# Kernel optimization log

Measured on AMD Instinct MI355X. Metric: run time of the kernel, lower is better.

Reference implementation:

```python
import jax, jax.numpy as jnp
import numpy as np

B, N, E = 4, 50000, 800000
C_IN, C_OUT, K = 64, 64, 3  # K = max_degree
AVG_DEG = 16.0


def setup_inputs() -> dict:
    key = jax.random.key(0)
    k1, k2, k3, k4, k5 = jax.random.split(key, 5)
    x = jax.random.normal(k1, (B, N, C_IN), dtype=jnp.float32)
    lap_rows = jax.random.randint(k2, (E,), 0, N)
    lap_cols = jax.random.randint(k3, (E,), 0, N)
    # scale so ||L|| stays O(1) and the Chebyshev recursion is stable
    lap_vals = jax.random.normal(k4, (E,), dtype=jnp.float32) / AVG_DEG
    weights = jax.random.normal(k5, (K + 1, C_IN, C_OUT), dtype=jnp.float32) * 0.1
    bias = jnp.full((C_OUT,), 0.1, dtype=jnp.float32)
    return dict(x=x, lap_rows=lap_rows, lap_cols=lap_cols,
                lap_vals=lap_vals, weights=weights, bias=bias)


def reference(x, lap_rows, lap_cols, lap_vals, weights, bias):
    # Sparse L @ X via edge list: gather source rows, scale, scatter-add to dest rows.
    def spmm_one(xb):  # xb: [N, C]
        return jax.ops.segment_sum(lap_vals[:, None] * xb[lap_cols], lap_rows,
                                   num_segments=N)

    spmm = jax.vmap(spmm_one)  # [B, N, C] -> [B, N, C]

    Tx0 = x
    out = jnp.einsum('bnc,co->bno', Tx0, weights[0])
    Tx1 = spmm(Tx0)
    out = out + jnp.einsum('bnc,co->bno', Tx1, weights[1])
    for k in range(2, K + 1):
        Tx2 = 2.0 * spmm(Tx1) - Tx0
        out = out + jnp.einsum('bnc,co->bno', Tx2, weights[k])
        Tx0, Tx1 = Tx1, Tx2
    return jax.nn.relu(out + bias)
```

## Files before the change

kernel.cpp:

```cpp
#include <hip/hip_runtime.h>


#define N_NODES 50000
#define N_EDGES 800000
#define BATCH 4
#define CH 64
#define BN (N_NODES * CH)
#define ROWS_TOTAL (BATCH * N_NODES)
#define NB 782
#define EPB 8192
#define SCT_BLOCKS ((N_EDGES + EPB - 1) / EPB)
#define TOTC (NB * SCT_BLOCKS)
#define SCAN2_BLOCKS ((TOTC + 1023) / 1024)

typedef unsigned int uint;
typedef unsigned short ushort;
typedef unsigned char uchar;
typedef __attribute__((ext_vector_type(8))) short short8;
typedef __attribute__((ext_vector_type(4))) float f32x4;

__device__ __forceinline__ uint pack_bf16(float lo, float hi) {
  uint a = __float_as_uint(lo);
  uint b = __float_as_uint(hi);
  a = (a + 0x7fffu + ((a >> 16) & 1u)) >> 16;
  b = (b + 0x7fffu + ((b >> 16) & 1u)) >> 16;
  return a | (b << 16);
}
__device__ __forceinline__ ushort bf16one(float x) {
  uint a = __float_as_uint(x);
  a = (a + 0x7fffu + ((a >> 16) & 1u)) >> 16;
  return (ushort)a;
}
__device__ __forceinline__ uint q_u8(float v, float inv) {
  return (uint)((int)rintf(v * inv) + 128) & 0xffu;
}

__global__ __launch_bounds__(1024) void bucket_hist(const int* __restrict__ rows,
                                                    int* __restrict__ bcounts) {
  __shared__ int h[NB];
  for (int b = threadIdx.x; b < NB; b += 1024) h[b] = 0;
  __syncthreads();
  int base_e = blockIdx.x * EPB;
#pragma unroll
  for (int j = 0; j < EPB / 1024; ++j) {
    int e = base_e + j * 1024 + threadIdx.x;
    if (e < N_EDGES) atomicAdd(&h[rows[e] >> 6], 1);
  }
  __syncthreads();
  for (int b = threadIdx.x; b < NB; b += 1024)
    bcounts[(size_t)b * SCT_BLOCKS + blockIdx.x] = h[b];
}

__global__ __launch_bounds__(1024) void partial2(const int* __restrict__ bc,
                                                 int* __restrict__ bsums) {
  int t = blockIdx.x * 1024 + threadIdx.x;
  int v = (t < TOTC) ? bc[t] : 0;
#pragma unroll
  for (int off = 1; off < 64; off <<= 1) v += __shfl_xor(v, off, 64);
  __shared__ int ws[16];
  if ((threadIdx.x & 63) == 0) ws[threadIdx.x >> 6] = v;
  __syncthreads();
  if (threadIdx.x < 16) {
    int s = ws[threadIdx.x];
#pragma unroll
    for (int off = 1; off < 16; off <<= 1) s += __shfl_xor(s, off, 64);
    if (threadIdx.x == 0) bsums[blockIdx.x] = s;
  }
}

__global__ __launch_bounds__(128) void scanb2(const int* __restrict__ bsums,
                                              int* __restrict__ boff) {
  __shared__ int s[128];
  int tid = threadIdx.x;
  int v = (tid < SCAN2_BLOCKS) ? bsums[tid] : 0;
  s[tid] = v;
  __syncthreads();
  for (int off = 1; off < 128; off <<= 1) {
    int t = (tid >= off) ? s[tid - off] : 0;
    __syncthreads();
    s[tid] += t;
    __syncthreads();
  }
  boff[tid] = s[tid] - v;
}

__global__ __launch_bounds__(1024) void expand2(const int* __restrict__ bc,
                                                const int* __restrict__ boff,
                                                int* __restrict__ bases) {
  int t = blockIdx.x * 1024 + threadIdx.x;
  int tid = threadIdx.x;
  int v = (t < TOTC) ? bc[t] : 0;
  __shared__ int s[1024];
  s[tid] = v;
  __syncthreads();
  for (int off = 1; off < 1024; off <<= 1) {
    int tv = (tid >= off) ? s[tid - off] : 0;
    __syncthreads();
    s[tid] += tv;
    __syncthreads();
  }
  if (t < TOTC) bases[t] = boff[blockIdx.x] + s[tid] - v;
}

__global__ __launch_bounds__(1024) void bucket_scatter(const int* __restrict__ rows,
                                                       const int* __restrict__ cols,
                                                       const float* __restrict__ vals,
                                                       const int* __restrict__ bases,
                                                       uint2* __restrict__ staging) {
  __shared__ int lcur[NB];
  for (int b = threadIdx.x; b < NB; b += 1024)
    lcur[b] = bases[(size_t)b * SCT_BLOCKS + blockIdx.x];
  __syncthreads();
  int base_e = blockIdx.x * EPB;
#pragma unroll
  for (int j = 0; j < EPB / 1024; ++j) {
    int e = base_e + j * 1024 + threadIdx.x;
    if (e < N_EDGES) {
      int r = rows[e];
      int pos = atomicAdd(&lcur[r >> 6], 1);
      staging[pos] = make_uint2((uint)cols[e] | ((uint)(r & 63) << 20),
                                __float_as_uint(vals[e]));
    }
  }
}

__global__ __launch_bounds__(256) void bucket_finalize(const int* __restrict__ bases,
                                                       const uint2* __restrict__ staging,
                                                       uint2* __restrict__ pairs,
                                                       int* __restrict__ row_start) {
  int b = blockIdx.x;
  int seg0 = bases[(size_t)b * SCT_BLOCKS];
  int seg1 = (b == NB - 1) ? N_EDGES : bases[(size_t)(b + 1) * SCT_BLOCKS];
  __shared__ int hist[64];
  __shared__ int cur[64];
  if (threadIdx.x < 64) hist[threadIdx.x] = 0;
  __syncthreads();
  for (int i = seg0 + threadIdx.x; i < seg1; i += 256)
    atomicAdd(&hist[staging[i].x >> 20], 1);
  __syncthreads();
  if (threadIdx.x < 64) {
    int v = hist[threadIdx.x];
    int sc = v;
#pragma unroll
    for (int off = 1; off < 64; off <<= 1) {
      int t = __shfl_up(sc, off, 64);
      if (threadIdx.x >= (unsigned)off) sc += t;
    }
    int start = seg0 + sc - v;
    cur[threadIdx.x] = start;
    int r = b * 64 + threadIdx.x;
    if (r < N_NODES) row_start[r] = start;
    if (r == N_NODES) row_start[N_NODES] = N_EDGES;
  }
  __syncthreads();
  for (int i = seg0 + threadIdx.x; i < seg1; i += 256) {
    uint2 eu = staging[i];
    int rl = eu.x >> 20;
    int pos = atomicAdd(&cur[rl], 1);
    pairs[pos] = make_uint2(eu.x & 0xFFFFFu, eu.y);
  }
}

__global__ __launch_bounds__(256) void wprep_kernel(const float* __restrict__ w,
                                                    ushort* __restrict__ wtT) {
  int t = blockIdx.x * 256 + threadIdx.x;
  if (t >= 64 * 256) return;
  int o = t >> 8, k = t & 255, m = k >> 6, c = k & 63;
  int idx = c * 64 + o;
  float v;
  if (m == 0)      v = w[idx] - w[2 * 4096 + idx];
  else if (m == 1) v = w[4096 + idx] - 3.0f * w[3 * 4096 + idx];
  else if (m == 2) v = 2.0f * w[2 * 4096 + idx];
  else             v = 4.0f * w[3 * 4096 + idx];
  wtT[t] = bf16one(v);
}

__global__ __launch_bounds__(256) void cvt_kernel(const float* __restrict__ in,
                                                  uint* __restrict__ xu8w,
                                                  float* __restrict__ xsc) {
  int node = blockIdx.x * 4 + (threadIdx.x >> 6);
  int lane = threadIdx.x & 63;
  int b = lane >> 4;
  int c4 = (lane & 15) * 4;
  float4 v = *reinterpret_cast<const float4*>(in + (size_t)b * BN + (size_t)node * 64 + c4);
  float mx = fmaxf(fmaxf(fabsf(v.x), fabsf(v.y)), fmaxf(fabsf(v.z), fabsf(v.w)));
#pragma unroll
  for (int off = 1; off < 64; off <<= 1) mx = fmaxf(mx, __shfl_xor(mx, off, 64));
  float inv = mx > 0.f ? 127.0f / mx : 0.f;
  uint w8 = q_u8(v.x, inv) | (q_u8(v.y, inv) << 8) |
            (q_u8(v.z, inv) << 16) | (q_u8(v.w, inv) << 24);
  xu8w[(size_t)node * 64 + b * 16 + (lane & 15)] = w8;
  if (lane == 0) xsc[node] = mx * (1.0f / 127.0f);
}

__device__ __forceinline__ void fma16_u8(float acc[16], float& sm, float m,
                                         const uint4& w) {
  const uint arr[4] = {w.x, w.y, w.z, w.w};
#pragma unroll
  for (int t = 0; t < 4; ++t) {
    uint u = arr[t];
    acc[t * 4 + 0] = fmaf(m, (float)(u & 0xffu),         acc[t * 4 + 0]);
    acc[t * 4 + 1] = fmaf(m, (float)((u >> 8) & 0xffu),  acc[t * 4 + 1]);
    acc[t * 4 + 2] = fmaf(m, (float)((u >> 16) & 0xffu), acc[t * 4 + 2]);
    acc[t * 4 + 3] = fmaf(m, (float)(u >> 24),           acc[t * 4 + 3]);
  }
  sm += m;
}

__device__ __forceinline__ void spmm_body(const int* __restrict__ row_start,
                                          const uint2* __restrict__ pairs,
                                          const uchar* __restrict__ src,
                                          const float* __restrict__ ssc,
                                          uchar* __restrict__ dst,
                                          float* __restrict__ dsc) {
  int row = blockIdx.x * 4 + (threadIdx.x >> 6);
  int lane = threadIdx.x & 63;
  int q = lane >> 4;
  int ql = lane & 15;
  const uchar* sb = src + ql * 16;
  int s = row_start[row], e = row_start[row + 1];
  float acc[16];
  float sm = 0.f;
#pragma unroll
  for (int j = 0; j < 16; ++j) acc[j] = 0.f;
  int i = s;
  for (; i + 7 < e; i += 8) {
    uint2 pa = pairs[i + q];
    uint2 pb = pairs[i + 4 + q];
    uint4 qa = *reinterpret_cast<const uint4*>(sb + (size_t)pa.x * 256);
    uint4 qb = *reinterpret_cast<const uint4*>(sb + (size_t)pb.x * 256);
    float ma = __uint_as_float(pa.y) * ssc[pa.x];
    float mb = __uint_as_float(pb.y) * ssc[pb.x];
    fma16_u8(acc, sm, ma, qa);
    fma16_u8(acc, sm, mb, qb);
  }
  for (; i < e; i += 4) {
    if (i + q < e) {
      uint2 p0 = pairs[i + q];
      uint4 q0 = *reinterpret_cast<const uint4*>(sb + (size_t)p0.x * 256);
      fma16_u8(acc, sm, __uint_as_float(p0.y) * ssc[p0.x], q0);
    }
  }
#pragma unroll
  for (int j = 0; j < 16; ++j) {
    acc[j] += __shfl_xor(acc[j], 16, 64);
    acc[j] += __shfl_xor(acc[j], 32, 64);
  }
  sm += __shfl_xor(sm, 16, 64);
  sm += __shfl_xor(sm, 32, 64);
#pragma unroll
  for (int j = 0; j < 16; ++j) acc[j] = fmaf(-128.f, sm, acc[j]);
  float mx = 0.f;
#pragma unroll
  for (int j = 0; j < 16; ++j) mx = fmaxf(mx, fabsf(acc[j]));
#pragma unroll
  for (int off = 1; off < 16; off <<= 1) mx = fmaxf(mx, __shfl_xor(mx, off, 64));
  if (lane < 16) {
    float inv = mx > 0.f ? 127.0f / mx : 0.f;
    uint w[4];
#pragma unroll
    for (int t = 0; t < 4; ++t) {
      w[t] = q_u8(acc[t * 4 + 0], inv) | (q_u8(acc[t * 4 + 1], inv) << 8) |
             (q_u8(acc[t * 4 + 2], inv) << 16) | (q_u8(acc[t * 4 + 3], inv) << 24);
    }
    *reinterpret_cast<uint4*>(dst + (size_t)row * 256 + ql * 16) =
        make_uint4(w[0], w[1], w[2], w[3]);
    if (lane == 0) dsc[row] = mx * (1.0f / 127.0f);
  }
}

__global__ __launch_bounds__(256) void spmm_s1(const int* __restrict__ rs,
                                               const uint2* __restrict__ pr,
                                               const uchar* __restrict__ src,
                                               const float* __restrict__ ssc,
                                               uchar* __restrict__ dst,
                                               float* __restrict__ dsc) {
  spmm_body(rs, pr, src, ssc, dst, dsc);
}
__global__ __launch_bounds__(256) void spmm_s2(const int* __restrict__ rs,
                                               const uint2* __restrict__ pr,
                                               const uchar* __restrict__ src,
                                               const float* __restrict__ ssc,
                                               uchar* __restrict__ dst,
                                               float* __restrict__ dsc) {
  spmm_body(rs, pr, src, ssc, dst, dsc);
}
__global__ __launch_bounds__(256) void spmm_s3(const int* __restrict__ rs,
                                               const uint2* __restrict__ pr,
                                               const uchar* __restrict__ src,
                                               const float* __restrict__ ssc,
                                               uchar* __restrict__ dst,
                                               float* __restrict__ dsc) {
  spmm_body(rs, pr, src, ssc, dst, dsc);
}

__device__ __forceinline__ short8 dequant8_u8(uint2 q, float sc, float nb) {
  float f0 = fmaf((float)(q.x & 0xffu),         sc, nb);
  float f1 = fmaf((float)((q.x >> 8) & 0xffu),  sc, nb);
  float f2 = fmaf((float)((q.x >> 16) & 0xffu), sc, nb);
  float f3 = fmaf((float)(q.x >> 24),           sc, nb);
  float f4 = fmaf((float)(q.y & 0xffu),         sc, nb);
  float f5 = fmaf((float)((q.y >> 8) & 0xffu),  sc, nb);
  float f6 = fmaf((float)((q.y >> 16) & 0xffu), sc, nb);
  float f7 = fmaf((float)(q.y >> 24),           sc, nb);
  uint4 v = make_uint4(pack_bf16(f0, f1), pack_bf16(f2, f3),
                       pack_bf16(f4, f5), pack_bf16(f6, f7));
  return __builtin_bit_cast(short8, v);
}

__global__ __launch_bounds__(256) void gemm4_mfma(
    const uchar* __restrict__ A0u8, const float* __restrict__ A0sc,
    const uchar* __restrict__ A1u8, const float* __restrict__ A1sc,
    const uchar* __restrict__ A2u8, const float* __restrict__ A2sc,
    const uchar* __restrict__ A3u8, const float* __restrict__ A3sc,
    const uint* __restrict__ wtT,
    const float* __restrict__ bias, float* __restrict__ out) {
  __shared__ uint WS[64 * 132];
  __shared__ float bias_s[64];
  for (int w = threadIdx.x; w < 8192; w += 256)
    WS[(w >> 7) * 132 + (w & 127)] = wtT[w];
  if (threadIdx.x < 64) bias_s[threadIdx.x] = bias[threadIdx.x];
  __syncthreads();

  const int lane = threadIdx.x & 63;
  const int wv = threadIdx.x >> 6;
  const int r0 = blockIdx.x * 64 + wv * 16;
  const int c16 = lane & 15;
  const int hi = lane >> 4;

  const int ar = r0 + c16;
  const size_t arow_b = (size_t)ar * 64 + hi * 8;
  const int nd = ar >> 2;
  const float sc0 = A0sc[nd];
  const float sc1 = A1sc[nd];
  const float sc2 = A2sc[nd];
  const float sc3 = A3sc[nd];

  f32x4 acc[4] = {{0.f, 0.f, 0.f, 0.f}, {0.f, 0.f, 0.f, 0.f},
                  {0.f, 0.f, 0.f, 0.f}, {0.f, 0.f, 0.f, 0.f}};

#pragma unroll
  for (int ks = 0; ks < 8; ++ks) {
    const int m = ks >> 1;
    const uchar* Au = (m == 0) ? A0u8 : (m == 1) ? A1u8 : (m == 2) ? A2u8 : A3u8;
    const float sc = (m == 0) ? sc0 : (m == 1) ? sc1 : (m == 2) ? sc2 : sc3;
    uint2 qv = *reinterpret_cast<const uint2*>(Au + arow_b + (ks & 1) * 32);
    short8 afrag = dequant8_u8(qv, sc, -128.f * sc);
#pragma unroll
    for (int nt = 0; nt < 4; ++nt) {
      uint4 bv = *reinterpret_cast<const uint4*>(
          &WS[(nt * 16 + c16) * 132 + ks * 16 + hi * 4]);
      short8 bfrag = __builtin_bit_cast(short8, bv);
      acc[nt] = __builtin_amdgcn_mfma_f32_16x16x32_bf16(afrag, bfrag, acc[nt], 0, 0, 0);
    }
  }

#pragma unroll
  for (int nt = 0; nt < 4; ++nt) {
#pragma unroll
    for (int i = 0; i < 4; ++i) {
      int row = r0 + hi * 4 + i;
      int node = row >> 2, b = row & 3;
      int col = nt * 16 + c16;
      float v = acc[nt][i] + bias_s[col];
      out[(size_t)b * BN + (size_t)node * 64 + col] = fmaxf(v, 0.f);
    }
  }
}

extern "C" void kernel_launch(void* const* d_in, const int* in_sizes, int n_in,
                              void* d_out, int out_size, void* d_ws, size_t ws_size,
                              hipStream_t stream) {
  const float* x        = (const float*)d_in[0];
  const int*   lap_rows = (const int*)d_in[1];
  const int*   lap_cols = (const int*)d_in[2];
  const float* lap_vals = (const float*)d_in[3];
  const float* weights  = (const float*)d_in[4];
  const float* bias     = (const float*)d_in[5];
  float* out = (float*)d_out;

  char* ws = (char*)d_ws;
  size_t off = 0;
  auto alloc = [&](size_t bytes) {
    void* p = ws + off;
    off += (bytes + 255) & ~(size_t)255;
    return p;
  };
  int*    bcounts     = (int*)alloc((size_t)TOTC * 4);
  int*    bases       = (int*)alloc((size_t)TOTC * 4);
  int*    bsums       = (int*)alloc((size_t)128 * 4);
  int*    boff        = (int*)alloc((size_t)128 * 4);
  int*    row_start   = (int*)alloc((size_t)(N_NODES + 1) * 4);
  uint2*  pairs       = (uint2*)alloc((size_t)N_EDGES * 8);
  uint2*  staging     = (uint2*)alloc((size_t)N_EDGES * 8);
  ushort* wtT         = (ushort*)alloc((size_t)64 * 256 * 2);
  uchar*  xu8         = (uchar*)alloc((size_t)N_NODES * 256);
  uchar*  S1u         = (uchar*)alloc((size_t)N_NODES * 256);
  uchar*  S2u         = (uchar*)alloc((size_t)N_NODES * 256);
  uchar*  S3u         = (uchar*)alloc((size_t)N_NODES * 256);
  float*  xsc         = (float*)alloc((size_t)N_NODES * 4);
  float*  S1sc        = (float*)alloc((size_t)N_NODES * 4);
  float*  S2sc        = (float*)alloc((size_t)N_NODES * 4);
  float*  S3sc        = (float*)alloc((size_t)N_NODES * 4);
  (void)ws_size; (void)in_sizes; (void)n_in; (void)out_size;

  wprep_kernel<<<64, 256, 0, stream>>>(weights, wtT);
  cvt_kernel<<<N_NODES / 4, 256, 0, stream>>>(x, (uint*)xu8, xsc);
  bucket_hist<<<SCT_BLOCKS, 1024, 0, stream>>>(lap_rows, bcounts);
  partial2<<<SCAN2_BLOCKS, 1024, 0, stream>>>(bcounts, bsums);
  scanb2<<<1, 128, 0, stream>>>(bsums, boff);
  expand2<<<SCAN2_BLOCKS, 1024, 0, stream>>>(bcounts, boff, bases);
  bucket_scatter<<<SCT_BLOCKS, 1024, 0, stream>>>(lap_rows, lap_cols, lap_vals,
                                                  bases, staging);
  bucket_finalize<<<NB, 256, 0, stream>>>(bases, staging, pairs, row_start);

  const int spmm_blocks = N_NODES / 4;

  spmm_s1<<<spmm_blocks, 256, 0, stream>>>(row_start, pairs, xu8, xsc, S1u, S1sc);
  spmm_s2<<<spmm_blocks, 256, 0, stream>>>(row_start, pairs, S1u, S1sc, S2u, S2sc);
  spmm_s3<<<spmm_blocks, 256, 0, stream>>>(row_start, pairs, S2u, S2sc, S3u, S3sc);
  gemm4_mfma<<<ROWS_TOTAL / 64, 256, 0, stream>>>(xu8, xsc, S1u, S1sc, S2u, S2sc,
                                                  S3u, S3sc, (const uint*)wtT,
                                                  bias, out);
}
```

Before: 189.1 us.

## Fuse third SpMM stage with the MFMA output GEMM

The last Chebyshev SpMM is merged with the final weight GEMM. Each block computes S3 for its 4 nodes, keeps the result in LDS as bf16 without quantizing it, and runs the MFMA over x, S1, S2 and the on-chip S3. This removes one launch plus the write and re-read of the quantized S3 buffer. In exchange, each wave computes only one 16-column output tile per block and reads weights straight from global/L2 rather than a shared LDS copy, so MFMA efficiency drops and weight traffic rises.

```diff
diff --git a/kernel.cpp b/kernel.cpp
--- a/kernel.cpp
+++ b/kernel.cpp
@@ -285,14 +285,6 @@
                                                float* __restrict__ dsc) {
   spmm_body(rs, pr, src, ssc, dst, dsc);
 }
-__global__ __launch_bounds__(256) void spmm_s3(const int* __restrict__ rs,
-                                               const uint2* __restrict__ pr,
-                                               const uchar* __restrict__ src,
-                                               const float* __restrict__ ssc,
-                                               uchar* __restrict__ dst,
-                                               float* __restrict__ dsc) {
-  spmm_body(rs, pr, src, ssc, dst, dsc);
-}
 
 __device__ __forceinline__ short8 dequant8_u8(uint2 q, float sc, float nb) {
   float f0 = fmaf((float)(q.x & 0xffu),         sc, nb);
@@ -308,63 +300,104 @@
   return __builtin_bit_cast(short8, v);
 }
 
-__global__ __launch_bounds__(256) void gemm4_mfma(
-    const uchar* __restrict__ A0u8, const float* __restrict__ A0sc,
-    const uchar* __restrict__ A1u8, const float* __restrict__ A1sc,
-    const uchar* __restrict__ A2u8, const float* __restrict__ A2sc,
-    const uchar* __restrict__ A3u8, const float* __restrict__ A3sc,
-    const uint* __restrict__ wtT,
-    const float* __restrict__ bias, float* __restrict__ out) {
-  __shared__ uint WS[64 * 132];
-  __shared__ float bias_s[64];
-  for (int w = threadIdx.x; w < 8192; w += 256)
-    WS[(w >> 7) * 132 + (w & 127)] = wtT[w];
-  if (threadIdx.x < 64) bias_s[threadIdx.x] = bias[threadIdx.x];
-  __syncthreads();
-
+__global__ __launch_bounds__(256) void spmm_s3_gemm(
+    const int* __restrict__ row_start, const uint2* __restrict__ pairs,
+    const uchar* __restrict__ xu8, const float* __restrict__ xsc,
+    const uchar* __restrict__ S1u, const float* __restrict__ S1sc,
+    const uchar* __restrict__ S2u, const float* __restrict__ S2sc,
+    const uint* __restrict__ wtT, const float* __restrict__ bias,
+    float* __restrict__ out) {
+  __shared__ uint S3L[16 * 36];
+  const int nb = blockIdx.x * 4;
+  const int wv = threadIdx.x >> 6;
+  const int row = nb + wv;
   const int lane = threadIdx.x & 63;
-  const int wv = threadIdx.x >> 6;
-  const int r0 = blockIdx.x * 64 + wv * 16;
+  const int q = lane >> 4;
+  const int ql = lane & 15;
+
+  const uchar* sb = S2u + ql * 16;
+  int s = row_start[row], e = row_start[row + 1];
+  float acc[16];
+  float sm = 0.f;
+#pragma unroll
+  for (int j = 0; j < 16; ++j) acc[j] = 0.f;
+  int i = s;
+  for (; i + 7 < e; i += 8) {
+    uint2 pa = pairs[i + q];
+    uint2 pb = pairs[i + 4 + q];
+    uint4 qa = *reinterpret_cast<const uint4*>(sb + (size_t)pa.x * 256);
+    uint4 qb = *reinterpret_cast<const uint4*>(sb + (size_t)pb.x * 256);
+    float ma = __uint_as_float(pa.y) * S2sc[pa.x];
+    float mb = __uint_as_float(pb.y) * S2sc[pb.x];
+    fma16_u8(acc, sm, ma, qa);
+    fma16_u8(acc, sm, mb, qb);
+  }
+  for (; i < e; i += 4) {
+    if (i + q < e) {
+      uint2 p0 = pairs[i + q];
+      uint4 q0 = *reinterpret_cast<const uint4*>(sb + (size_t)p0.x * 256);
+      fma16_u8(acc, sm, __uint_as_float(p0.y) * S2sc[p0.x], q0);
+    }
+  }
+#pragma unroll
+  for (int j = 0; j < 16; ++j) {
+    acc[j] += __shfl_xor(acc[j], 16, 64);
+    acc[j] += __shfl_xor(acc[j], 32, 64);
+  }
+  sm += __shfl_xor(sm, 16, 64);
+  sm += __shfl_xor(sm, 32, 64);
+#pragma unroll
+  for (int j = 0; j < 16; ++j) acc[j] = fmaf(-128.f, sm, acc[j]);
+
+  if (lane < 16) {
+    int r = wv * 4 + (ql >> 2);
+    int w0 = (ql & 3) * 8;
+    uint wb[8];
+#pragma unroll
+    for (int t = 0; t < 8; ++t) wb[t] = pack_bf16(acc[2 * t], acc[2 * t + 1]);
+    *reinterpret_cast<uint4*>(&S3L[r * 36 + w0]) =
+        make_uint4(wb[0], wb[1], wb[2], wb[3]);
+    *reinterpret_cast<uint4*>(&S3L[r * 36 + w0 + 4]) =
+        make_uint4(wb[4], wb[5], wb[6], wb[7]);
+  }
+  __syncthreads();
+
   const int c16 = lane & 15;
   const int hi = lane >> 4;
-
-  const int ar = r0 + c16;
-  const size_t arow_b = (size_t)ar * 64 + hi * 8;
-  const int nd = ar >> 2;
-  const float sc0 = A0sc[nd];
-  const float sc1 = A1sc[nd];
-  const float sc2 = A2sc[nd];
-  const float sc3 = A3sc[nd];
-
-  f32x4 acc[4] = {{0.f, 0.f, 0.f, 0.f}, {0.f, 0.f, 0.f, 0.f},
-                  {0.f, 0.f, 0.f, 0.f}, {0.f, 0.f, 0.f, 0.f}};
-
+  const int gnode = nb + (c16 >> 2);
+  const int bb = c16 & 3;
+  const size_t abase = (size_t)gnode * 256 + bb * 64 + hi * 8;
+  const float sc0 = xsc[gnode];
+  const float sc1 = S1sc[gnode];
+  const float sc2 = S2sc[gnode];
+  const int ocol = wv * 16 + c16;
+
+  f32x4 accd = {0.f, 0.f, 0.f, 0.f};
 #pragma unroll
   for (int ks = 0; ks < 8; ++ks) {
-    const int m = ks >> 1;
-    const uchar* Au = (m == 0) ? A0u8 : (m == 1) ? A1u8 : (m == 2) ? A2u8 : A3u8;
-    const float sc = (m == 0) ? sc0 : (m == 1) ? sc1 : (m == 2) ? sc2 : sc3;
-    uint2 qv = *reinterpret_cast<const uint2*>(Au + arow_b + (ks & 1) * 32);
-    short8 afrag = dequant8_u8(qv, sc, -128.f * sc);
-#pragma unroll
-    for (int nt = 0; nt < 4; ++nt) {
-      uint4 bv = *reinterpret_cast<const uint4*>(
-          &WS[(nt * 16 + c16) * 132 + ks * 16 + hi * 4]);
-      short8 bfrag = __builtin_bit_cast(short8, bv);
-      acc[nt] = __builtin_amdgcn_mfma_f32_16x16x32_bf16(afrag, bfrag, acc[nt], 0, 0, 0);
-    }
-  }
-
-#pragma unroll
-  for (int nt = 0; nt < 4; ++nt) {
-#pragma unroll
-    for (int i = 0; i < 4; ++i) {
-      int row = r0 + hi * 4 + i;
-      int node = row >> 2, b = row & 3;
-      int col = nt * 16 + c16;
-      float v = acc[nt][i] + bias_s[col];
-      out[(size_t)b * BN + (size_t)node * 64 + col] = fmaxf(v, 0.f);
-    }
+    const int m = ks >> 1, kk = ks & 1;
+    short8 afrag;
+    if (m == 3) {
+      uint4 av = *reinterpret_cast<const uint4*>(&S3L[c16 * 36 + kk * 16 + hi * 4]);
+      afrag = __builtin_bit_cast(short8, av);
+    } else {
+      const uchar* Au = (m == 0) ? xu8 : (m == 1) ? S1u : S2u;
+      const float sc = (m == 0) ? sc0 : (m == 1) ? sc1 : sc2;
+      uint2 qv = *reinterpret_cast<const uint2*>(Au + abase + kk * 32);
+      afrag = dequant8_u8(qv, sc, -128.f * sc);
+    }
+    uint4 bv = *reinterpret_cast<const uint4*>(wtT + (size_t)ocol * 128 +
+                                               ks * 16 + hi * 4);
+    short8 bfrag = __builtin_bit_cast(short8, bv);
+    accd = __builtin_amdgcn_mfma_f32_16x16x32_bf16(afrag, bfrag, accd, 0, 0, 0);
+  }
+
+  const float bs = bias[ocol];
+#pragma unroll
+  for (int i2 = 0; i2 < 4; ++i2) {
+    int r = hi * 4 + i2;
+    int gn = nb + (r >> 2), b2 = r & 3;
+    out[(size_t)b2 * BN + (size_t)gn * 64 + ocol] = fmaxf(accd[i2] + bs, 0.f);
   }
 }
 
@@ -397,11 +430,9 @@
   uchar*  xu8         = (uchar*)alloc((size_t)N_NODES * 256);
   uchar*  S1u         = (uchar*)alloc((size_t)N_NODES * 256);
   uchar*  S2u         = (uchar*)alloc((size_t)N_NODES * 256);
-  uchar*  S3u         = (uchar*)alloc((size_t)N_NODES * 256);
   float*  xsc         = (float*)alloc((size_t)N_NODES * 4);
   float*  S1sc        = (float*)alloc((size_t)N_NODES * 4);
   float*  S2sc        = (float*)alloc((size_t)N_NODES * 4);
-  float*  S3sc        = (float*)alloc((size_t)N_NODES * 4);
   (void)ws_size; (void)in_sizes; (void)n_in; (void)out_size;
 
   wprep_kernel<<<64, 256, 0, stream>>>(weights, wtT);
@@ -418,8 +449,7 @@
 
   spmm_s1<<<spmm_blocks, 256, 0, stream>>>(row_start, pairs, xu8, xsc, S1u, S1sc);
   spmm_s2<<<spmm_blocks, 256, 0, stream>>>(row_start, pairs, S1u, S1sc, S2u, S2sc);
-  spmm_s3<<<spmm_blocks, 256, 0, stream>>>(row_start, pairs, S2u, S2sc, S3u, S3sc);
-  gemm4_mfma<<<ROWS_TOTAL / 64, 256, 0, stream>>>(xu8, xsc, S1u, S1sc, S2u, S2sc,
-                                                  S3u, S3sc, (const uint*)wtT,
-                                                  bias, out);
-}
+  spmm_s3_gemm<<<spmm_blocks, 256, 0, stream>>>(row_start, pairs, xu8, xsc,
+                                                S1u, S1sc, S2u, S2sc,
+                                                (const uint*)wtT, bias, out);
+}
```

After: 214.7 us. +13.5%, slower.
